# Kernel tuning notes

Measured on AMD Instinct MI355X. Metric: run time of the kernel, lower is better.

The kernel has to match this reference:

```python
import jax, jax.numpy as jnp
import numpy as np

EMBED_DIM = 1024
NUM_HEADS = 16
HEAD_DIM = EMBED_DIM // NUM_HEADS
MAX_SEQ_LEN = 2048
B, T = 2, 2048


def setup_inputs() -> dict:
    key = jax.random.key(0)
    ks = jax.random.split(key, 12)
    d = EMBED_DIM
    s = lambda fan_in: 1.0 / np.sqrt(fan_in)
    return {
        "x": jax.random.normal(ks[0], (B, T, d), dtype=jnp.float32),
        "ln1_g": jnp.ones((d,), jnp.float32),
        "ln1_b": jnp.zeros((d,), jnp.float32),
        "w_attn": jax.random.normal(ks[1], (d, 3 * d), jnp.float32) * s(d),
        "b_attn": jnp.zeros((3 * d,), jnp.float32),
        "w_proj": jax.random.normal(ks[2], (d, d), jnp.float32) * s(d),
        "b_proj": jnp.zeros((d,), jnp.float32),
        "ln2_g": jnp.ones((d,), jnp.float32),
        "ln2_b": jnp.zeros((d,), jnp.float32),
        "w_fc": jax.random.normal(ks[3], (d, 4 * d), jnp.float32) * s(d),
        "b_fc": jnp.zeros((4 * d,), jnp.float32),
        "w_fc2": jax.random.normal(ks[4], (4 * d, d), jnp.float32) * s(4 * d),
        "b_fc2": jnp.zeros((d,), jnp.float32),
    }


def _layernorm(x, g, b, eps=1e-5):
    mu = jnp.mean(x, axis=-1, keepdims=True)
    var = jnp.var(x, axis=-1, keepdims=True)
    return (x - mu) * jax.lax.rsqrt(var + eps) * g + b


def _attention(x, w_attn, b_attn, w_proj, b_proj):
    b, t, c = x.shape
    qkv = x @ w_attn + b_attn  # [B,T,3C]
    q, k, v = jnp.split(qkv, 3, axis=-1)
    # [B,T,C] -> [B,H,T,Dh]
    rs = lambda a: a.reshape(b, t, NUM_HEADS, HEAD_DIM).transpose(0, 2, 1, 3)
    q, k, v = rs(q), rs(k), rs(v)
    wei = jnp.einsum("bhqd,bhkd->bhqk", q, k) * (HEAD_DIM ** -0.5)
    causal = jnp.tril(jnp.ones((t, t), bool))
    wei = jnp.where(causal, wei, -jnp.inf)
    wei = jax.nn.softmax(wei, axis=-1)  # attn_dropout is identity in eval mode
    out = jnp.einsum("bhqk,bhkd->bhqd", wei, v)
    out = out.transpose(0, 2, 1, 3).reshape(b, t, c)
    return out @ w_proj + b_proj  # resid_dropout identity in eval mode


def _ffn(x, w_fc, b_fc, w_fc2, b_fc2):
    h = jax.nn.gelu(x @ w_fc + b_fc, approximate=False)
    return h @ w_fc2 + b_fc2  # dropout identity in eval mode


def reference(x, ln1_g, ln1_b, w_attn, b_attn, w_proj, b_proj,
              ln2_g, ln2_b, w_fc, b_fc, w_fc2, b_fc2):
    x = x + _attention(_layernorm(x, ln1_g, ln1_b), w_attn, b_attn, w_proj, b_proj)
    x = x + _ffn(_layernorm(x, ln2_g, ln2_b), w_fc, b_fc, w_fc2, b_fc2)
    return x
```

## Files before the change

### kernel.cpp

```cpp
#include <hip/hip_runtime.h>

#define EMBED 1024
#define THREE_EMBED 3072
#define HEADS 16
#define HDIM 64
#define SEQ 2048
#define BATCH 2
#define MTOT 4096

typedef short bf16x8 __attribute__((ext_vector_type(8)));
typedef float f32x4 __attribute__((ext_vector_type(4)));

#define MFMA16(a, b, c) __builtin_amdgcn_mfma_f32_16x16x32_bf16(a, b, c, 0, 0, 0)

__device__ __forceinline__ unsigned short f2bf(float f) {
  union { float f; unsigned int u; } v; v.f = f;
  unsigned int r = v.u + 0x7fffu + ((v.u >> 16) & 1u);
  return (unsigned short)(r >> 16);
}

__device__ __forceinline__ void gload_lds16(const unsigned short* g, unsigned short* l) {
  __builtin_amdgcn_global_load_lds(
      (const __attribute__((address_space(1))) void*)g,
      (__attribute__((address_space(3))) void*)l, 16, 0, 0);
}

__device__ __forceinline__ void wait_vm0_barrier() {
  asm volatile("s_waitcnt vmcnt(0)" ::: "memory");
  __builtin_amdgcn_s_barrier();
}

template <int N>
__device__ __forceinline__ void wait_vmcnt() {
  if constexpr (N == 0) asm volatile("s_waitcnt vmcnt(0)" ::: "memory");
  else if constexpr (N == 1) asm volatile("s_waitcnt vmcnt(1)" ::: "memory");
  else if constexpr (N == 2) asm volatile("s_waitcnt vmcnt(2)" ::: "memory");
  else if constexpr (N == 3) asm volatile("s_waitcnt vmcnt(3)" ::: "memory");
  else if constexpr (N == 4) asm volatile("s_waitcnt vmcnt(4)" ::: "memory");
  else if constexpr (N == 6) asm volatile("s_waitcnt vmcnt(6)" ::: "memory");
  else if constexpr (N == 8) asm volatile("s_waitcnt vmcnt(8)" ::: "memory");
}

__device__ __forceinline__ void open_phase_barrier() {
  __builtin_amdgcn_s_barrier();
  __builtin_amdgcn_sched_barrier(0);
}

__global__ __launch_bounds__(256) void k_transpose_bf16(
    const float* __restrict__ in, unsigned short* __restrict__ out, int K, int N) {
  __shared__ float t[32][33];
  int tx = threadIdx.x & 31, ty = threadIdx.x >> 5;
  int n0 = blockIdx.x * 32, k0 = blockIdx.y * 32;
#pragma unroll
  for (int i = 0; i < 32; i += 8)
    t[ty + i][tx] = in[(size_t)(k0 + ty + i) * N + n0 + tx];
  __syncthreads();
#pragma unroll
  for (int i = 0; i < 32; i += 8)
    out[(size_t)(n0 + ty + i) * K + k0 + tx] = f2bf(t[tx][ty + i]);
}

__global__ __launch_bounds__(256) void k_transpose_v(
    const unsigned short* __restrict__ qkv, unsigned short* __restrict__ Vt) {
  __shared__ unsigned short t[32][33];
  int tx = threadIdx.x & 31, ty = threadIdx.x >> 5;
  int t0 = blockIdx.x * 32;
  int d0 = (blockIdx.y & 1) * 32;
  int bh = blockIdx.y >> 1;
  int b = bh >> 4, h = bh & 15;
  const unsigned short* src = qkv + (size_t)b * SEQ * THREE_EMBED + 2 * EMBED + h * HDIM;
#pragma unroll
  for (int i = 0; i < 32; i += 8)
    t[ty + i][tx] = src[(size_t)(t0 + ty + i) * THREE_EMBED + d0 + tx];
  __syncthreads();
  unsigned short* dst = Vt + (size_t)bh * HDIM * SEQ;
#pragma unroll
  for (int i = 0; i < 32; i += 8)
    dst[(size_t)(d0 + ty + i) * SEQ + t0 + tx] = t[tx][ty + i];
}

__global__ __launch_bounds__(256) void k_layernorm(
    const float* __restrict__ x, const float* __restrict__ g,
    const float* __restrict__ b, unsigned short* __restrict__ out) {
  int row = blockIdx.x;
  int tid = threadIdx.x;
  const float4 xv = *(const float4*)(x + (size_t)row * EMBED + tid * 4);
  float s = xv.x + xv.y + xv.z + xv.w;
  float sq = xv.x * xv.x + xv.y * xv.y + xv.z * xv.z + xv.w * xv.w;
#pragma unroll
  for (int off = 1; off < 64; off <<= 1) {
    s += __shfl_xor(s, off);
    sq += __shfl_xor(sq, off);
  }
  __shared__ float red[8];
  int w = tid >> 6;
  if ((tid & 63) == 0) { red[w] = s; red[4 + w] = sq; }
  __syncthreads();
  s = red[0] + red[1] + red[2] + red[3];
  sq = red[4] + red[5] + red[6] + red[7];
  float mu = s * (1.0f / EMBED);
  float var = sq * (1.0f / EMBED) - mu * mu;
  float rs = rsqrtf(var + 1e-5f);
  float xs[4] = {xv.x, xv.y, xv.z, xv.w};
  unsigned short o[4];
#pragma unroll
  for (int c = 0; c < 4; c++) {
    int col = tid * 4 + c;
    o[c] = f2bf((xs[c] - mu) * rs * g[col] + b[col]);
  }
  *(ushort4*)(out + (size_t)row * EMBED + tid * 4) = *(const ushort4*)o;
}

template <int EPI>
__global__ __launch_bounds__(512, 2) void k_gemm8(
    const unsigned short* __restrict__ A, const unsigned short* __restrict__ Bt,
    const float* __restrict__ bias, const float* __restrict__ resid,
    float* __restrict__ outf, unsigned short* __restrict__ outb,
    int M, int N, int K) {
  __shared__ unsigned short lA[2][16384];
  __shared__ unsigned short lB[2][16384];
  int tid = threadIdx.x;
  int nwg = gridDim.x * gridDim.y;
  int bid = blockIdx.y * gridDim.x + blockIdx.x;
  int swz = (bid & 7) * (nwg >> 3) + (bid >> 3);
  int m0 = (swz / gridDim.x) * 256, n0 = (swz % gridDim.x) * 256;
  int lane = tid & 63, w = tid >> 6;
  int lr = lane & 15, lg = lane >> 4;
  int warow = (w >> 2) * 64;
  int wbrow = (w & 3) * 32;
  int rx = lr & 7;
  int colk[2] = {(lg ^ rx) * 8, ((4 + lg) ^ rx) * 8};
  f32x4 acc[8][4] = {};
  int swzk = ((lane & 7) ^ ((lane >> 3) & 7)) * 8;
  const unsigned short* gA[2];
  const unsigned short* gB[2];
#pragma unroll
  for (int i = 0; i < 2; i++) {
    int chrow = (w * 2 + i) * 8 + (lane >> 3);
    gA[i] = A + (size_t)(m0 + chrow) * K + swzk;
    gB[i] = Bt + (size_t)(n0 + chrow) * K + swzk;
  }
  int NT = K >> 6;
  auto stageA = [&](int h, int kt, int buf) {
    size_t goff = (size_t)(h * 128) * K + (size_t)kt * 64;
    int lo = h * 8192 + w * 1024;
    gload_lds16(gA[0] + goff, &lA[buf][lo]);
    gload_lds16(gA[1] + goff, &lA[buf][lo + 512]);
  };
  auto stageB = [&](int h, int kt, int buf) {
    size_t goff = (size_t)(h * 128) * K + (size_t)kt * 64;
    int lo = h * 8192 + w * 1024;
    gload_lds16(gB[0] + goff, &lB[buf][lo]);
    gload_lds16(gB[1] + goff, &lB[buf][lo + 512]);
  };
  bf16x8 aX[4][2], aY[4][2], b0[2][2], b1[2][2];
  auto rdA = [&](int buf, int mh, bf16x8 (&dst)[4][2]) {
#pragma unroll
    for (int ii = 0; ii < 4; ii++) {
      int ra = mh * 128 + warow + ii * 16 + lr;
#pragma unroll
      for (int ks = 0; ks < 2; ks++)
        dst[ii][ks] = *(const bf16x8*)&lA[buf][ra * 64 + colk[ks]];
    }
  };
  auto rdB = [&](int buf, int nh, bf16x8 (&dst)[2][2]) {
#pragma unroll
    for (int jj = 0; jj < 2; jj++) {
      int rb = nh * 128 + wbrow + jj * 16 + lr;
#pragma unroll
      for (int ks = 0; ks < 2; ks++)
        dst[jj][ks] = *(const bf16x8*)&lB[buf][rb * 64 + colk[ks]];
    }
  };
  auto mf = [&](int mh, int nh, bf16x8 (&aa)[4][2], bf16x8 (&bb)[2][2]) {
    __builtin_amdgcn_s_setprio(1);
#pragma unroll
    for (int ii = 0; ii < 4; ii++)
#pragma unroll
      for (int jj = 0; jj < 2; jj++)
#pragma unroll
        for (int ks = 0; ks < 2; ks++)
          acc[mh * 4 + ii][nh * 2 + jj] =
              MFMA16(aa[ii][ks], bb[jj][ks], acc[mh * 4 + ii][nh * 2 + jj]);
    __builtin_amdgcn_s_setprio(0);
  };
  stageA(0, 0, 0); stageB(0, 0, 0); stageB(1, 0, 0); stageA(1, 0, 0);
  wait_vmcnt<6>();
  open_phase_barrier();
  rdA(0, 0, aX);
  for (int t = 0; t < NT - 1; t++) {
    int cur = t & 1, nxt = cur ^ 1;
    stageA(0, t + 1, nxt);
    wait_vmcnt<4>();
    open_phase_barrier();
    rdB(cur, 0, b0);
    rdB(cur, 1, b1);
    mf(0, 0, aX, b0);
    stageB(0, t + 1, nxt);
    wait_vmcnt<4>();
    open_phase_barrier();
    rdA(cur, 1, aY);
    mf(0, 1, aX, b1);
    stageB(1, t + 1, nxt);
    wait_vmcnt<4>();
    open_phase_barrier();
    mf(1, 1, aY, b1);
    stageA(1, t + 1, nxt);
    wait_vmcnt<4>();
    open_phase_barrier();
    rdA(nxt, 0, aX);
    mf(1, 0, aY, b0);
  }
  {
    int cur = (NT - 1) & 1;
    wait_vmcnt<2>();
    open_phase_barrier();
    rdB(cur, 0, b0);
    rdB(cur, 1, b1);
    mf(0, 0, aX, b0);
    wait_vmcnt<0>();
    open_phase_barrier();
    rdA(cur, 1, aY);
    mf(0, 1, aX, b1);
    mf(1, 1, aY, b1);
    mf(1, 0, aY, b0);
  }
#pragma unroll
  for (int i = 0; i < 8; i++) {
#pragma unroll
    for (int j = 0; j < 4; j++) {
      int col = n0 + (j >> 1) * 128 + wbrow + (j & 1) * 16 + lr;
      float bv = bias[col];
#pragma unroll
      for (int r = 0; r < 4; r++) {
        int row = m0 + (i >> 2) * 128 + warow + (i & 3) * 16 + lg * 4 + r;
        float v = acc[i][j][r] + bv;
        size_t idx = (size_t)row * N + col;
        if constexpr (EPI == 0) {
          outb[idx] = f2bf(v);
        } else if constexpr (EPI == 1) {
          outf[idx] = v + resid[idx];
        } else {
          float gv = 0.5f * v * (1.0f + erff(v * 0.70710678118654752f));
          outb[idx] = f2bf(gv);
        }
      }
    }
  }
}

template <int EPI>
__global__ __launch_bounds__(256) void k_gemmN(
    const unsigned short* __restrict__ A, const unsigned short* __restrict__ Bt,
    const float* __restrict__ bias, const float* __restrict__ resid,
    float* __restrict__ outf, unsigned short* __restrict__ outb,
    int M, int N, int K) {
  __shared__ unsigned short lA[3][128 * 64];
  __shared__ unsigned short lB[3][64 * 64];
  int tid = threadIdx.x;
  int nwg = gridDim.x * gridDim.y;
  int bid = blockIdx.y * gridDim.x + blockIdx.x;
  int swz = (bid & 7) * (nwg >> 3) + (bid >> 3);
  int m0 = (swz / gridDim.x) * 128, n0 = (swz % gridDim.x) * 64;
  int lane = tid & 63, w = tid >> 6;
  int wm = w * 32;
  int lr = lane & 15, lg = lane >> 4;
  int rx = lr & 7;
  int colk[2] = {(lg ^ rx) * 8, ((4 + lg) ^ rx) * 8};
  f32x4 acc[2][4] = {};
  int swzk = ((lane & 7) ^ ((lane >> 3) & 7)) * 8;
  const unsigned short* gsrc[6];
  int loff[6];
  bool isa[6];
#pragma unroll
  for (int c0 = 0; c0 < 6; c0++) {
    int c = w * 6 + c0;
    if (c < 16) {
      int row = c * 8 + (lane >> 3);
      gsrc[c0] = A + (size_t)(m0 + row) * K + swzk;
      loff[c0] = c * 512;
      isa[c0] = true;
    } else {
      int row = (c - 16) * 8 + (lane >> 3);
      gsrc[c0] = Bt + (size_t)(n0 + row) * K + swzk;
      loff[c0] = (c - 16) * 512;
      isa[c0] = false;
    }
  }
  auto stage = [&](int k0, int buf) {
#pragma unroll
    for (int c0 = 0; c0 < 6; c0++)
      gload_lds16(gsrc[c0] + k0, isa[c0] ? &lA[buf][loff[c0]] : &lB[buf][loff[c0]]);
  };
  auto compute = [&](int buf) {
    bf16x8 af[2][2], bf[4][2];
#pragma unroll
    for (int i = 0; i < 2; i++)
#pragma unroll
      for (int ks = 0; ks < 2; ks++)
        af[i][ks] = *(const bf16x8*)&lA[buf][(wm + i * 16 + lr) * 64 + colk[ks]];
#pragma unroll
    for (int j = 0; j < 4; j++)
#pragma unroll
      for (int ks = 0; ks < 2; ks++)
        bf[j][ks] = *(const bf16x8*)&lB[buf][(j * 16 + lr) * 64 + colk[ks]];
    __builtin_amdgcn_s_setprio(1);
#pragma unroll
    for (int i = 0; i < 2; i++)
#pragma unroll
      for (int j = 0; j < 4; j++)
#pragma unroll
        for (int ks = 0; ks < 2; ks++)
          acc[i][j] = MFMA16(af[i][ks], bf[j][ks], acc[i][j]);
    __builtin_amdgcn_s_setprio(0);
  };
  int nt = K >> 6;
  stage(0, 0);
  stage(64, 1);
  wait_vmcnt<6>();
  __builtin_amdgcn_s_barrier();
  int c0 = 0, c1 = 1, c2 = 2;
  for (int t = 0; t < nt - 2; t++) {
    stage((t + 2) * 64, c2);
    compute(c0);
    wait_vmcnt<6>();
    __builtin_amdgcn_s_barrier();
    int tmp = c0; c0 = c1; c1 = c2; c2 = tmp;
  }
  compute(c0);
  wait_vmcnt<0>();
  __builtin_amdgcn_s_barrier();
  compute(c1);
#pragma unroll
  for (int i = 0; i < 2; i++) {
#pragma unroll
    for (int j = 0; j < 4; j++) {
      int colb = n0 + j * 16 + lr;
      float bv = bias[colb];
#pragma unroll
      for (int r = 0; r < 4; r++) {
        int row = m0 + wm + i * 16 + lg * 4 + r;
        float v = acc[i][j][r] + bv;
        size_t idx = (size_t)row * N + colb;
        if constexpr (EPI == 0) {
          outb[idx] = f2bf(v);
        } else if constexpr (EPI == 1) {
          outf[idx] = v + resid[idx];
        } else {
          float gv = 0.5f * v * (1.0f + erff(v * 0.70710678118654752f));
          outb[idx] = f2bf(gv);
        }
      }
    }
  }
}

__global__ __launch_bounds__(256) void k_attention(
    const unsigned short* __restrict__ qkv, const unsigned short* __restrict__ Vt,
    unsigned short* __restrict__ out) {
  __shared__ unsigned short lK[2][64 * 64];
  __shared__ unsigned short lV[2][64 * 64];
  __shared__ unsigned short lP[4][16][72];
  int bid = blockIdx.x;
  int i = bid >> 3;
  int qt = 31 - (i >> 2);
  int bh = (bid & 7) * 4 + (i & 3);
  int b = bh >> 4, h = bh & 15;
  int tid = threadIdx.x, lane = tid & 63, w = tid >> 6;
  int lr = lane & 15, lg = lane >> 4;
  const unsigned short* base = qkv + (size_t)b * SEQ * THREE_EMBED + h * HDIM;
  const unsigned short* Kb = base + EMBED;
  const unsigned short* Vb = Vt + (size_t)bh * HDIM * SEQ;
  int q0 = qt * 64 + w * 16;
  bf16x8 qf[2];
  {
    int qrow = q0 + lr;
    qf[0] = *(const bf16x8*)(base + (size_t)qrow * THREE_EMBED + lg * 8);
    qf[1] = *(const bf16x8*)(base + (size_t)qrow * THREE_EMBED + 32 + lg * 8);
  }
  bf16x8 ones;
  {
    short o1 = 0x3F80;
#pragma unroll
    for (int j = 0; j < 8; j++) ones[j] = o1;
  }
  f32x4 o[4] = {};
  f32x4 osum = {};
  float m_[4] = {-INFINITY, -INFINITY, -INFINITY, -INFINITY};
  int srow = lane >> 3;
  int scol = ((lane & 7) ^ (lane >> 3)) * 8;
  const float SCL = 0.125f * 1.4426950408889634f;
  int nkv = qt + 1;
  auto stage = [&](int kt, int cur) {
#pragma unroll
    for (int c = 0; c < 2; c++) {
      int chunk = w * 2 + c;
      int row = chunk * 8 + srow;
      gload_lds16(Kb + (size_t)(kt * 64 + row) * THREE_EMBED + scol, &lK[cur][chunk * 512]);
      gload_lds16(Vb + (size_t)row * SEQ + kt * 64 + scol, &lV[cur][chunk * 512]);
    }
  };
  stage(0, 0);
  wait_vm0_barrier();
  int cur = 0;
  for (int kt = 0; kt < nkv; kt++) {
    if (kt + 1 < nkv) stage(kt + 1, cur ^ 1);
    __builtin_amdgcn_s_setprio(1);
    f32x4 s[4];
#pragma unroll
    for (int ct = 0; ct < 4; ct++) {
      int krow = ct * 16 + lr;
      int sw = (krow & 7) << 3;
      bf16x8 k0 = *(const bf16x8*)&lK[cur][krow * 64 + ((lg * 8) ^ sw)];
      bf16x8 k1 = *(const bf16x8*)&lK[cur][krow * 64 + ((32 + lg * 8) ^ sw)];
      f32x4 z = {};
      z = MFMA16(qf[0], k0, z);
      s[ct] = MFMA16(qf[1], k1, z);
    }
    __builtin_amdgcn_s_setprio(0);
    bool maskt = (kt * 64 + 63 > q0);
    float pm[4] = {-INFINITY, -INFINITY, -INFINITY, -INFINITY};
#pragma unroll
    for (int ct = 0; ct < 4; ct++) {
#pragma unroll
      for (int r = 0; r < 4; r++) {
        float sv = s[ct][r] * SCL;
        if (maskt) {
          int kg = kt * 64 + ct * 16 + lr;
          int qg = q0 + lg * 4 + r;
          if (kg > qg) sv = -INFINITY;
        }
        s[ct][r] = sv;
        pm[r] = fmaxf(pm[r], sv);
      }
    }
    float dm = fmaxf(fmaxf(pm[0] - m_[0], pm[1] - m_[1]),
                     fmaxf(pm[2] - m_[2], pm[3] - m_[3]));
    if (!__all(dm <= 8.0f)) {
#pragma unroll
      for (int r = 0; r < 4; r++) {
        float mx = pm[r];
        mx = fmaxf(mx, __shfl_xor(mx, 1));
        mx = fmaxf(mx, __shfl_xor(mx, 2));
        mx = fmaxf(mx, __shfl_xor(mx, 4));
        mx = fmaxf(mx, __shfl_xor(mx, 8));
        float mn = fmaxf(m_[r], mx);
        float al = exp2f(m_[r] - mn);
        m_[r] = mn;
        osum[r] *= al;
#pragma unroll
        for (int dt = 0; dt < 4; dt++) o[dt][r] *= al;
      }
    }
#pragma unroll
    for (int ct = 0; ct < 4; ct++)
#pragma unroll
      for (int r = 0; r < 4; r++)
        lP[w][lg * 4 + r][ct * 16 + lr] = f2bf(exp2f(s[ct][r] - m_[r]));
    __builtin_amdgcn_s_setprio(1);
#pragma unroll
    for (int ks = 0; ks < 2; ks++) {
      bf16x8 pf = *(const bf16x8*)&lP[w][lr][ks * 32 + lg * 8];
      osum = MFMA16(pf, ones, osum);
#pragma unroll
      for (int dt = 0; dt < 4; dt++) {
        int vrow = dt * 16 + lr;
        int sw = (vrow & 7) << 3;
        bf16x8 vf = *(const bf16x8*)&lV[cur][vrow * 64 + ((ks * 32 + lg * 8) ^ sw)];
        o[dt] = MFMA16(pf, vf, o[dt]);
      }
    }
    __builtin_amdgcn_s_setprio(0);
    wait_vm0_barrier();
    cur ^= 1;
  }
#pragma unroll
  for (int dt = 0; dt < 4; dt++)
#pragma unroll
    for (int r = 0; r < 4; r++) {
      int row = q0 + lg * 4 + r;
      float val = o[dt][r] / osum[r];
      out[(size_t)(b * SEQ + row) * EMBED + h * HDIM + dt * 16 + lr] = f2bf(val);
    }
}

extern "C" void kernel_launch(void* const* d_in, const int* in_sizes, int n_in,
                              void* d_out, int out_size, void* d_ws, size_t ws_size,
                              hipStream_t stream) {
  const float* x      = (const float*)d_in[0];
  const float* ln1_g  = (const float*)d_in[1];
  const float* ln1_b  = (const float*)d_in[2];
  const float* w_attn = (const float*)d_in[3];
  const float* b_attn = (const float*)d_in[4];
  const float* w_proj = (const float*)d_in[5];
  const float* b_proj = (const float*)d_in[6];
  const float* ln2_g  = (const float*)d_in[7];
  const float* ln2_b  = (const float*)d_in[8];
  const float* w_fc   = (const float*)d_in[9];
  const float* b_fc   = (const float*)d_in[10];
  const float* w_fc2  = (const float*)d_in[11];
  const float* b_fc2  = (const float*)d_in[12];
  float* outp = (float*)d_out;

  char* ws = (char*)d_ws;
  unsigned short* wT_attn = (unsigned short*)(ws);
  unsigned short* wT_proj = (unsigned short*)(ws + 6291456);
  unsigned short* wT_fc   = (unsigned short*)(ws + 8388608);
  unsigned short* wT_fc2  = (unsigned short*)(ws + 16777216);
  unsigned short* buf1    = (unsigned short*)(ws + 25165824);
  float*          x1      = (float*)(ws + 33554432);
  unsigned short* Vt      = (unsigned short*)(ws + 33554432);
  unsigned short* qkv_h   = (unsigned short*)(ws + 50331648);

  dim3 blk(256);
  k_transpose_bf16<<<dim3(3072 / 32, 1024 / 32), blk, 0, stream>>>(w_attn, wT_attn, 1024, 3072);
  k_transpose_bf16<<<dim3(1024 / 32, 1024 / 32), blk, 0, stream>>>(w_proj, wT_proj, 1024, 1024);
  k_transpose_bf16<<<dim3(4096 / 32, 1024 / 32), blk, 0, stream>>>(w_fc, wT_fc, 1024, 4096);
  k_transpose_bf16<<<dim3(1024 / 32, 4096 / 32), blk, 0, stream>>>(w_fc2, wT_fc2, 4096, 1024);
  k_layernorm<<<dim3(MTOT), blk, 0, stream>>>(x, ln1_g, ln1_b, buf1);
  k_gemm8<0><<<dim3(THREE_EMBED / 256, MTOT / 256), dim3(512), 0, stream>>>(
      buf1, wT_attn, b_attn, nullptr, nullptr, qkv_h, MTOT, THREE_EMBED, EMBED);
  k_transpose_v<<<dim3(SEQ / 32, 2 * BATCH * HEADS), blk, 0, stream>>>(qkv_h, Vt);
  k_attention<<<dim3(1024), blk, 0, stream>>>(qkv_h, Vt, buf1);
  k_gemmN<1><<<dim3(EMBED / 64, MTOT / 128), blk, 0, stream>>>(
      buf1, wT_proj, b_proj, x, x1, nullptr, MTOT, EMBED, EMBED);
  k_layernorm<<<dim3(MTOT), blk, 0, stream>>>(x1, ln2_g, ln2_b, buf1);
  k_gemm8<2><<<dim3(4 * EMBED / 256, MTOT / 256), dim3(512), 0, stream>>>(
      buf1, wT_fc, b_fc, nullptr, nullptr, qkv_h, MTOT, 4 * EMBED, EMBED);
  k_gemmN<1><<<dim3(EMBED / 64, MTOT / 128), blk, 0, stream>>>(
      qkv_h, wT_fc2, b_fc2, x1, outp, nullptr, MTOT, EMBED, 4 * EMBED);
}
```

Measured before the change: 241.8 us.

## Process 128 query rows per attention block, two 16-row slices per wave

Each attention block now covers 128 query rows instead of 64, and each wave handles 32 rows as two 16-row MFMA slices. The grid shrinks from 1024 to 512 blocks. Every K/V tile staged into LDS is reused by twice as many queries, which halves global K/V traffic and staging per query. In exchange, register pressure and LDS use for P rise, there are fewer blocks to fill the CUs, and waves whose rows lie entirely before a diagonal tile skip its compute but still wait at the barrier.

```diff
diff --git a/kernel.cpp b/kernel.cpp
--- a/kernel.cpp
+++ b/kernel.cpp
@@ -360,10 +360,10 @@
     unsigned short* __restrict__ out) {
   __shared__ unsigned short lK[2][64 * 64];
   __shared__ unsigned short lV[2][64 * 64];
-  __shared__ unsigned short lP[4][16][72];
+  __shared__ unsigned short lP[4][32][72];
   int bid = blockIdx.x;
   int i = bid >> 3;
-  int qt = 31 - (i >> 2);
+  int qt = 15 - (i >> 2);
   int bh = (bid & 7) * 4 + (i & 3);
   int b = bh >> 4, h = bh & 15;
   int tid = threadIdx.x, lane = tid & 63, w = tid >> 6;
@@ -371,12 +371,13 @@
   const unsigned short* base = qkv + (size_t)b * SEQ * THREE_EMBED + h * HDIM;
   const unsigned short* Kb = base + EMBED;
   const unsigned short* Vb = Vt + (size_t)bh * HDIM * SEQ;
-  int q0 = qt * 64 + w * 16;
-  bf16x8 qf[2];
-  {
-    int qrow = q0 + lr;
-    qf[0] = *(const bf16x8*)(base + (size_t)qrow * THREE_EMBED + lg * 8);
-    qf[1] = *(const bf16x8*)(base + (size_t)qrow * THREE_EMBED + 32 + lg * 8);
+  int q0 = qt * 128 + w * 32;
+  bf16x8 qf[2][2];
+#pragma unroll
+  for (int qs = 0; qs < 2; qs++) {
+    int qrow = q0 + qs * 16 + lr;
+    qf[qs][0] = *(const bf16x8*)(base + (size_t)qrow * THREE_EMBED + lg * 8);
+    qf[qs][1] = *(const bf16x8*)(base + (size_t)qrow * THREE_EMBED + 32 + lg * 8);
   }
   bf16x8 ones;
   {
@@ -384,13 +385,17 @@
 #pragma unroll
     for (int j = 0; j < 8; j++) ones[j] = o1;
   }
-  f32x4 o[4] = {};
-  f32x4 osum = {};
-  float m_[4] = {-INFINITY, -INFINITY, -INFINITY, -INFINITY};
+  f32x4 o[2][4] = {};
+  f32x4 osum[2] = {};
+  float m_[2][4];
+#pragma unroll
+  for (int qs = 0; qs < 2; qs++)
+#pragma unroll
+    for (int r = 0; r < 4; r++) m_[qs][r] = -INFINITY;
   int srow = lane >> 3;
   int scol = ((lane & 7) ^ (lane >> 3)) * 8;
   const float SCL = 0.125f * 1.4426950408889634f;
-  int nkv = qt + 1;
+  int nkv = 2 * qt + 2;
   auto stage = [&](int kt, int cur) {
 #pragma unroll
     for (int c = 0; c < 2; c++) {
@@ -405,83 +410,111 @@
   int cur = 0;
   for (int kt = 0; kt < nkv; kt++) {
     if (kt + 1 < nkv) stage(kt + 1, cur ^ 1);
-    __builtin_amdgcn_s_setprio(1);
-    f32x4 s[4];
-#pragma unroll
-    for (int ct = 0; ct < 4; ct++) {
-      int krow = ct * 16 + lr;
-      int sw = (krow & 7) << 3;
-      bf16x8 k0 = *(const bf16x8*)&lK[cur][krow * 64 + ((lg * 8) ^ sw)];
-      bf16x8 k1 = *(const bf16x8*)&lK[cur][krow * 64 + ((32 + lg * 8) ^ sw)];
-      f32x4 z = {};
-      z = MFMA16(qf[0], k0, z);
-      s[ct] = MFMA16(qf[1], k1, z);
-    }
-    __builtin_amdgcn_s_setprio(0);
-    bool maskt = (kt * 64 + 63 > q0);
-    float pm[4] = {-INFINITY, -INFINITY, -INFINITY, -INFINITY};
-#pragma unroll
-    for (int ct = 0; ct < 4; ct++) {
-#pragma unroll
-      for (int r = 0; r < 4; r++) {
-        float sv = s[ct][r] * SCL;
-        if (maskt) {
-          int kg = kt * 64 + ct * 16 + lr;
-          int qg = q0 + lg * 4 + r;
-          if (kg > qg) sv = -INFINITY;
-        }
-        s[ct][r] = sv;
-        pm[r] = fmaxf(pm[r], sv);
-      }
-    }
-    float dm = fmaxf(fmaxf(pm[0] - m_[0], pm[1] - m_[1]),
-                     fmaxf(pm[2] - m_[2], pm[3] - m_[3]));
-    if (!__all(dm <= 8.0f)) {
-#pragma unroll
-      for (int r = 0; r < 4; r++) {
-        float mx = pm[r];
-        mx = fmaxf(mx, __shfl_xor(mx, 1));
-        mx = fmaxf(mx, __shfl_xor(mx, 2));
-        mx = fmaxf(mx, __shfl_xor(mx, 4));
-        mx = fmaxf(mx, __shfl_xor(mx, 8));
-        float mn = fmaxf(m_[r], mx);
-        float al = exp2f(m_[r] - mn);
-        m_[r] = mn;
-        osum[r] *= al;
-#pragma unroll
-        for (int dt = 0; dt < 4; dt++) o[dt][r] *= al;
-      }
-    }
-#pragma unroll
-    for (int ct = 0; ct < 4; ct++)
-#pragma unroll
-      for (int r = 0; r < 4; r++)
-        lP[w][lg * 4 + r][ct * 16 + lr] = f2bf(exp2f(s[ct][r] - m_[r]));
-    __builtin_amdgcn_s_setprio(1);
-#pragma unroll
-    for (int ks = 0; ks < 2; ks++) {
-      bf16x8 pf = *(const bf16x8*)&lP[w][lr][ks * 32 + lg * 8];
-      osum = MFMA16(pf, ones, osum);
-#pragma unroll
-      for (int dt = 0; dt < 4; dt++) {
-        int vrow = dt * 16 + lr;
-        int sw = (vrow & 7) << 3;
-        bf16x8 vf = *(const bf16x8*)&lV[cur][vrow * 64 + ((ks * 32 + lg * 8) ^ sw)];
-        o[dt] = MFMA16(pf, vf, o[dt]);
-      }
-    }
-    __builtin_amdgcn_s_setprio(0);
+    if (q0 + 31 >= kt * 64) {
+      __builtin_amdgcn_s_setprio(1);
+      f32x4 s[2][4];
+#pragma unroll
+      for (int ct = 0; ct < 4; ct++) {
+        int krow = ct * 16 + lr;
+        int sw = (krow & 7) << 3;
+        bf16x8 k0 = *(const bf16x8*)&lK[cur][krow * 64 + ((lg * 8) ^ sw)];
+        bf16x8 k1 = *(const bf16x8*)&lK[cur][krow * 64 + ((32 + lg * 8) ^ sw)];
+#pragma unroll
+        for (int qs = 0; qs < 2; qs++) {
+          f32x4 z = {};
+          z = MFMA16(qf[qs][0], k0, z);
+          s[qs][ct] = MFMA16(qf[qs][1], k1, z);
+        }
+      }
+      __builtin_amdgcn_s_setprio(0);
+      bool maskt = (kt * 64 + 63 > q0);
+      float pm[2][4];
+#pragma unroll
+      for (int qs = 0; qs < 2; qs++)
+#pragma unroll
+        for (int r = 0; r < 4; r++) pm[qs][r] = -INFINITY;
+#pragma unroll
+      for (int qs = 0; qs < 2; qs++) {
+#pragma unroll
+        for (int ct = 0; ct < 4; ct++) {
+#pragma unroll
+          for (int r = 0; r < 4; r++) {
+            float sv = s[qs][ct][r] * SCL;
+            if (maskt) {
+              int kg = kt * 64 + ct * 16 + lr;
+              int qg = q0 + qs * 16 + lg * 4 + r;
+              if (kg > qg) sv = -INFINITY;
+            }
+            s[qs][ct][r] = sv;
+            pm[qs][r] = fmaxf(pm[qs][r], sv);
+          }
+        }
+      }
+      float dm = -INFINITY;
+#pragma unroll
+      for (int qs = 0; qs < 2; qs++)
+#pragma unroll
+        for (int r = 0; r < 4; r++) dm = fmaxf(dm, pm[qs][r] - m_[qs][r]);
+      if (!__all(dm <= 8.0f)) {
+#pragma unroll
+        for (int qs = 0; qs < 2; qs++) {
+#pragma unroll
+          for (int r = 0; r < 4; r++) {
+            float mx = pm[qs][r];
+            mx = fmaxf(mx, __shfl_xor(mx, 1));
+            mx = fmaxf(mx, __shfl_xor(mx, 2));
+            mx = fmaxf(mx, __shfl_xor(mx, 4));
+            mx = fmaxf(mx, __shfl_xor(mx, 8));
+            float mn = fmaxf(m_[qs][r], mx);
+            float al = exp2f(m_[qs][r] - mn);
+            m_[qs][r] = mn;
+            osum[qs][r] *= al;
+#pragma unroll
+            for (int dt = 0; dt < 4; dt++) o[qs][dt][r] *= al;
+          }
+        }
+      }
+#pragma unroll
+      for (int qs = 0; qs < 2; qs++)
+#pragma unroll
+        for (int ct = 0; ct < 4; ct++)
+#pragma unroll
+          for (int r = 0; r < 4; r++)
+            lP[w][qs * 16 + lg * 4 + r][ct * 16 + lr] = f2bf(exp2f(s[qs][ct][r] - m_[qs][r]));
+      __builtin_amdgcn_s_setprio(1);
+#pragma unroll
+      for (int ks = 0; ks < 2; ks++) {
+        bf16x8 pf[2];
+#pragma unroll
+        for (int qs = 0; qs < 2; qs++) {
+          pf[qs] = *(const bf16x8*)&lP[w][qs * 16 + lr][ks * 32 + lg * 8];
+          osum[qs] = MFMA16(pf[qs], ones, osum[qs]);
+        }
+#pragma unroll
+        for (int dt = 0; dt < 4; dt++) {
+          int vrow = dt * 16 + lr;
+          int sw = (vrow & 7) << 3;
+          bf16x8 vf = *(const bf16x8*)&lV[cur][vrow * 64 + ((ks * 32 + lg * 8) ^ sw)];
+#pragma unroll
+          for (int qs = 0; qs < 2; qs++)
+            o[qs][dt] = MFMA16(pf[qs], vf, o[qs][dt]);
+        }
+      }
+      __builtin_amdgcn_s_setprio(0);
+    }
     wait_vm0_barrier();
     cur ^= 1;
   }
 #pragma unroll
-  for (int dt = 0; dt < 4; dt++)
-#pragma unroll
-    for (int r = 0; r < 4; r++) {
-      int row = q0 + lg * 4 + r;
-      float val = o[dt][r] / osum[r];
-      out[(size_t)(b * SEQ + row) * EMBED + h * HDIM + dt * 16 + lr] = f2bf(val);
-    }
+  for (int qs = 0; qs < 2; qs++)
+#pragma unroll
+    for (int dt = 0; dt < 4; dt++)
+#pragma unroll
+      for (int r = 0; r < 4; r++) {
+        int row = q0 + qs * 16 + lg * 4 + r;
+        float val = o[qs][dt][r] / osum[qs][r];
+        out[(size_t)(b * SEQ + row) * EMBED + h * HDIM + dt * 16 + lr] = f2bf(val);
+      }
 }
 
 extern "C" void kernel_launch(void* const* d_in, const int* in_sizes, int n_in,
@@ -521,7 +554,7 @@
   k_gemm8<0><<<dim3(THREE_EMBED / 256, MTOT / 256), dim3(512), 0, stream>>>(
       buf1, wT_attn, b_attn, nullptr, nullptr, qkv_h, MTOT, THREE_EMBED, EMBED);
   k_transpose_v<<<dim3(SEQ / 32, 2 * BATCH * HEADS), blk, 0, stream>>>(qkv_h, Vt);
-  k_attention<<<dim3(1024), blk, 0, stream>>>(qkv_h, Vt, buf1);
+  k_attention<<<dim3(512), blk, 0, stream>>>(qkv_h, Vt, buf1);
   k_gemmN<1><<<dim3(EMBED / 64, MTOT / 128), blk, 0, stream>>>(
       buf1, wT_proj, b_proj, x, x1, nullptr, MTOT, EMBED, EMBED);
   k_layernorm<<<dim3(MTOT), blk, 0, stream>>>(x1, ln2_g, ln2_b, buf1);
```

Result: slower. 265.5 us (+9.8%).
